# Kernel optimization log

Measured on AMD Instinct MI355X. Metric: run time of the kernel, lower is better.

The kernel has to match this reference:

```python
import jax, jax.numpy as jnp
import numpy as np

# Config (matches init_kwargs)
IN_CH = 128
HID = 128
HEADS = 1
B, H, W = 8, 192, 192


def setup_inputs() -> dict:
    key = jax.random.key(0)
    ks = jax.random.split(key, 10)
    s = 0.05
    x = jax.random.normal(ks[0], (B, IN_CH, H, W), dtype=jnp.float32)
    # 1x1 conv weights stored as (out, in); bias (out,)
    Wq = jax.random.normal(ks[1], (HID, IN_CH), dtype=jnp.float32) * s
    bq = jax.random.normal(ks[2], (HID,), dtype=jnp.float32) * s
    Wk = jax.random.normal(ks[3], (HID, IN_CH), dtype=jnp.float32) * s
    bk = jax.random.normal(ks[4], (HID,), dtype=jnp.float32) * s
    Wv = jax.random.normal(ks[5], (HID, IN_CH), dtype=jnp.float32) * s
    bv = jax.random.normal(ks[6], (HID,), dtype=jnp.float32) * s
    Wo = jax.random.normal(ks[7], (IN_CH, HID), dtype=jnp.float32) * s
    bo = jax.random.normal(ks[8], (IN_CH,), dtype=jnp.float32) * s
    gamma = jax.random.normal(ks[9], (1,), dtype=jnp.float32) * 0.5
    return {"x": x, "Wq": Wq, "bq": bq, "Wk": Wk, "bk": bk,
            "Wv": Wv, "bv": bv, "Wo": Wo, "bo": bo, "gamma": gamma}


def _conv1x1(x, Wt, b):
    # x: (B, Cin, H, W); Wt: (Cout, Cin) -> (B, Cout, H, W)
    return jnp.einsum('oc,bchw->bohw', Wt, x) + b[None, :, None, None]


def reference(x, Wq, bq, Wk, bk, Wv, bv, Wo, bo, gamma):
    b, c, h, w = x.shape
    n = h * w
    d = HID // HEADS
    # q/k/v: (B, hidden, H, W) -> view(B, d, heads, N) -> (B*heads, d, N)
    def proj(Wt, bias):
        y = _conv1x1(x, Wt, bias).reshape(b, d, HEADS, n)
        return jnp.transpose(y, (0, 2, 1, 3)).reshape(b * HEADS, d, n)
    q = proj(Wq, bq)
    k = proj(Wk, bk)
    v = proj(Wv, bv)
    # NOTE: energy is d x d (channel attention), contracted over N. No scale.
    energy = jnp.einsum('bdn,ben->bde', q, k)        # (B*heads, d, d)
    attention = jax.nn.softmax(energy, axis=-1)
    attn_out = jnp.einsum('bde,ben->bdn', attention, v)  # (B*heads, d, N)
    attn_out = attn_out.reshape(b, HEADS, d, n)
    attn_out = jnp.transpose(attn_out, (0, 2, 1, 3)).reshape(b, HID, h, w)
    attn_out = _conv1x1(attn_out, Wo, bo)
    return gamma * attn_out + x
```

## Files before the change

kernel.cpp:

```cpp
#include <hip/hip_runtime.h>
#include <cstdint>
#include <cstddef>

#define NB  8
#define NC  128
#define NHW 36864

#define GOFF  0
#define SOFF  131072
#define TOFF  132096
#define ROFF  133120
#define CVOFF 264192
#define MBOFF 265216

typedef __attribute__((ext_vector_type(8))) short short8;
typedef __attribute__((ext_vector_type(4))) float f32x4;

static __device__ __forceinline__ f32x4 zero4(){ f32x4 v = {0.f,0.f,0.f,0.f}; return v; }

static __device__ __forceinline__ short bfbits(float f){
    union { __bf16 b; short s; } u; u.b = (__bf16)f; return u.s;
}
static __device__ __forceinline__ void cv2(float f, short& hb, short& lb){
    union { __bf16 b; short s; } u;
    u.b = (__bf16)f; hb = u.s;
    float hf = (float)u.b;
    u.b = (__bf16)(f - hf); lb = u.s;
}
static __device__ __forceinline__ float cv8(f32x4 v0, f32x4 v1, short8& h, short8& l){
    float ss = 0.f;
#pragma unroll
    for (int j=0;j<4;j++){
        short hb, lb;
        cv2(v0[j], hb, lb); h[j]   = hb; l[j]   = lb;
        cv2(v1[j], hb, lb); h[4+j] = hb; l[4+j] = lb;
        ss += v0[j] + v1[j];
    }
    return ss;
}

__global__ __launch_bounds__(256) void k_zero(float* __restrict__ p){
    const int i = (blockIdx.x*256 + threadIdx.x)*4;
    *(f32x4*)(p + i) = zero4();
}

#define GNT 36
#define GLDH 5120

__global__ __launch_bounds__(512) void k_gram(const float* __restrict__ x,
                                              float* __restrict__ G,
                                              float* __restrict__ svec){
    __shared__ short Ls[2][2][GLDH];
    const int b     = blockIdx.y;
    const int chunk = blockIdx.x;
    const int tid   = threadIdx.x;
    const int wid   = tid >> 6, lane = tid & 63;
    const int l16   = lane & 15, lgi = lane >> 4;
    const int sr    = tid >> 2;
    const int sc    = (tid & 3) * 8;

    const float* xs = x + (size_t)b*NC*NHW + (size_t)sr*NHW + chunk*1152 + sc;

    float srow = 0.f;
    f32x4 acc[8];
#pragma unroll
    for (int g=0;g<8;g++) acc[g] = zero4();

    const int ra = (wid*16 + l16)*40 + lgi*8;

    {
        f32x4 v0 = *(const f32x4*)(xs);
        f32x4 v1 = *(const f32x4*)(xs+4);
        short8 h0,l0;
        srow += cv8(v0,v1,h0,l0);
        *(short8*)&Ls[0][0][sr*40 + sc] = h0;
        *(short8*)&Ls[0][1][sr*40 + sc] = l0;
    }
    __syncthreads();

    for (int t=0; t<GNT-1; ++t){
        const float* p = xs + (t+1)*32;
        f32x4 v0 = *(const f32x4*)(p);
        f32x4 v1 = *(const f32x4*)(p+4);
        __builtin_amdgcn_sched_barrier(0);

        {
            const short* Lh = Ls[t&1][0];
            const short* Ll = Ls[t&1][1];
            short8 hA = *(const short8*)(Lh + ra);
            short8 lA = *(const short8*)(Ll + ra);
#pragma unroll
            for (int g=0; g<8; g++){
                const int rb = (g*16 + l16)*40 + lgi*8;
                short8 hg  = *(const short8*)(Lh + rb);
                short8 lg2 = *(const short8*)(Ll + rb);
                acc[g] = __builtin_amdgcn_mfma_f32_16x16x32_bf16(hA, hg,  acc[g], 0,0,0);
                acc[g] = __builtin_amdgcn_mfma_f32_16x16x32_bf16(hA, lg2, acc[g], 0,0,0);
                acc[g] = __builtin_amdgcn_mfma_f32_16x16x32_bf16(lA, hg,  acc[g], 0,0,0);
            }
        }

        {
            short8 h0,l0;
            srow += cv8(v0,v1,h0,l0);
            *(short8*)&Ls[(t+1)&1][0][sr*40 + sc] = h0;
            *(short8*)&Ls[(t+1)&1][1][sr*40 + sc] = l0;
        }
        __syncthreads();
    }

    {
        const short* Lh = Ls[(GNT-1)&1][0];
        const short* Ll = Ls[(GNT-1)&1][1];
        short8 hA = *(const short8*)(Lh + ra);
        short8 lA = *(const short8*)(Ll + ra);
#pragma unroll
        for (int g=0; g<8; g++){
            const int rb = (g*16 + l16)*40 + lgi*8;
            short8 hg  = *(const short8*)(Lh + rb);
            short8 lg2 = *(const short8*)(Ll + rb);
            acc[g] = __builtin_amdgcn_mfma_f32_16x16x32_bf16(hA, hg,  acc[g], 0,0,0);
            acc[g] = __builtin_amdgcn_mfma_f32_16x16x32_bf16(hA, lg2, acc[g], 0,0,0);
            acc[g] = __builtin_amdgcn_mfma_f32_16x16x32_bf16(lA, hg,  acc[g], 0,0,0);
        }
    }

    float* Gb = G + (size_t)b*NC*NC;
#pragma unroll
    for (int g=0;g<8;g++){
#pragma unroll
        for (int r=0;r<4;r++){
            atomicAdd(&Gb[(size_t)(wid*16 + lgi*4 + r)*NC + g*16 + l16], acc[g][r]);
        }
    }
    srow += __shfl_xor(srow, 1);
    srow += __shfl_xor(srow, 2);
    if ((tid & 3) == 0) atomicAdd(&svec[b*NC + sr], srow);
}

__global__ __launch_bounds__(256) void k_energyav(const float* __restrict__ G,
        const float* __restrict__ svec,
        const float* __restrict__ Wq, const float* __restrict__ bq,
        const float* __restrict__ Wk, const float* __restrict__ bk,
        const float* __restrict__ bv, const float* __restrict__ Wv,
        float* __restrict__ R, float* __restrict__ tvec){
    const int b  = blockIdx.y;
    const int d0 = blockIdx.x * 16;
    const int tid = threadIdx.x;
    const int d  = tid & 15;
    const int ec = tid >> 4;

    __shared__ float Ps[16][128];
    __shared__ float Es[16][128];
    __shared__ float red[16][16];
    __shared__ float rowmax[16];
    __shared__ float rowsum[16];
    __shared__ float qs[16];

    const float* Wqrow = Wq + (size_t)(d0 + d)*NC;
    const float* sb = svec + b*NC;
#pragma unroll
    for (int i=0;i<8;i++){
        const int c = ec*8 + i;
        const float* Grow = G + ((size_t)b*NC + c)*NC;
        float a = 0.f;
        for (int c4=0;c4<32;c4++){
            f32x4 g4 = *(const f32x4*)(Grow + c4*4);
            f32x4 w4 = *(const f32x4*)(Wqrow + c4*4);
            a += g4[0]*w4[0] + g4[1]*w4[1] + g4[2]*w4[2] + g4[3]*w4[3];
        }
        Ps[d][c] = a;
    }
    if (ec == 0){
        float a = 0.f;
        for (int c4=0;c4<32;c4++){
            f32x4 w4 = *(const f32x4*)(Wqrow + c4*4);
            f32x4 s4 = *(const f32x4*)(sb + c4*4);
            a += w4[0]*s4[0] + w4[1]*s4[1] + w4[2]*s4[2] + w4[3]*s4[3];
        }
        qs[d] = a;
    }
    __syncthreads();
    const float bqd = bq[d0+d];
#pragma unroll
    for (int i=0;i<8;i++){
        const int e = ec*8 + i;
        const float* Wkrow = Wk + (size_t)e*NC;
        float ea = 0.f, ks = 0.f;
        for (int c4=0;c4<32;c4++){
            f32x4 w4 = *(const f32x4*)(Wkrow + c4*4);
            f32x4 p4 = *(const f32x4*)(&Ps[d][c4*4]);
            f32x4 s4 = *(const f32x4*)(sb + c4*4);
            ea += w4[0]*p4[0]+w4[1]*p4[1]+w4[2]*p4[2]+w4[3]*p4[3];
            ks += w4[0]*s4[0]+w4[1]*s4[1]+w4[2]*s4[2]+w4[3]*s4[3];
        }
        const float bke = bk[e];
        Es[d][e] = ea + bke*qs[d] + bqd*ks + (float)NHW*bqd*bke;
    }
    float m8 = -3.4e38f;
#pragma unroll
    for (int i=0;i<8;i++) m8 = fmaxf(m8, Es[d][ec*8+i]);
    red[d][ec] = m8;
    __syncthreads();
    if (tid < 16){
        float m = red[tid][0];
        for (int j=1;j<16;j++) m = fmaxf(m, red[tid][j]);
        rowmax[tid] = m;
    }
    __syncthreads();
    const float rm = rowmax[d];
    float s8 = 0.f;
#pragma unroll
    for (int i=0;i<8;i++){
        float ex = expf(Es[d][ec*8+i] - rm);
        Es[d][ec*8+i] = ex;
        s8 += ex;
    }
    red[d][ec] = s8;
    __syncthreads();
    if (tid < 16){
        float sm = 0.f;
        for (int j=0;j<16;j++) sm += red[tid][j];
        rowsum[tid] = sm;
    }
    __syncthreads();
    const float inv = 1.f / rowsum[d];
    float ta = 0.f;
#pragma unroll
    for (int i=0;i<8;i++){
        const int e = ec*8 + i;
        float av = Es[d][e] * inv;
        Es[d][e] = av;
        ta += av * bv[e];
    }
    red[d][ec] = ta;
    __syncthreads();
    if (tid < 16){
        float sm = 0.f;
        for (int j=0;j<16;j++) sm += red[tid][j];
        tvec[b*NC + d0 + tid] = sm;
    }
    const int c0 = ec*8;
    float racc[8];
#pragma unroll
    for (int i=0;i<8;i++) racc[i]=0.f;
    for (int e=0;e<NC;e++){
        const float av = Es[d][e];
        const float* wv = Wv + (size_t)e*NC + c0;
        f32x4 w0 = *(const f32x4*)wv;
        f32x4 w1 = *(const f32x4*)(wv+4);
        racc[0]+=av*w0[0]; racc[1]+=av*w0[1]; racc[2]+=av*w0[2]; racc[3]+=av*w0[3];
        racc[4]+=av*w1[0]; racc[5]+=av*w1[1]; racc[6]+=av*w1[2]; racc[7]+=av*w1[3];
    }
    float* Rrow = R + ((size_t)b*NC + d0 + d)*NC + c0;
#pragma unroll
    for (int i=0;i<8;i++) Rrow[i] = racc[i];
}

__global__ __launch_bounds__(256) void k_om(const float* __restrict__ R,
        const float* __restrict__ Wo, const float* __restrict__ bo,
        const float* __restrict__ tvec, const float* __restrict__ gamma,
        short* __restrict__ Mb_, float* __restrict__ cvg){
    const int b = blockIdx.y, o0 = blockIdx.x*16;
    const int tid = threadIdx.x, o = tid&15, cc = tid>>4;
    const int c0 = cc*8;
    const float* Worow = Wo + (size_t)(o0+o)*NC;
    const float* tb = tvec + b*NC;
    float a[8];
#pragma unroll
    for (int i=0;i<8;i++) a[i]=0.f;
    float cv = 0.f;
    for (int dd=0; dd<NC; dd++){
        const float wv = Worow[dd];
        const float* r = R + ((size_t)b*NC + dd)*NC + c0;
        f32x4 r0 = *(const f32x4*)r;
        f32x4 r1 = *(const f32x4*)(r+4);
        a[0]+=wv*r0[0]; a[1]+=wv*r0[1]; a[2]+=wv*r0[2]; a[3]+=wv*r0[3];
        a[4]+=wv*r1[0]; a[5]+=wv*r1[1]; a[6]+=wv*r1[2]; a[7]+=wv*r1[3];
        cv += wv*tb[dd];
    }
    const float gm = gamma[0];
    const int c   = o0 + o;
    const int cg  = c >> 4;
    const int kst = cc >> 2, lgv = cc & 3;
    const size_t idx = ((((size_t)b*8 + cg)*4 + kst)*64 + (lgv*16 + (c & 15)))*8;
    short8 hh;
#pragma unroll
    for (int i=0;i<8;i++){
        float val = gm*a[i] + ((c0 + i) == c ? 1.f : 0.f);
        hh[i] = bfbits(val);
    }
    *(short8*)(Mb_ + idx) = hh;
    if (cc == 0) cvg[b*NC + c] = gm*(cv + bo[c]);
}

__global__ __launch_bounds__(256, 4) void k_final(const float* __restrict__ x,
        const short* __restrict__ Mb_, const float* __restrict__ cvg,
        float* __restrict__ out){
    __shared__ short Xt[NC*128];
    const int b   = blockIdx.y;
    const int n0  = blockIdx.x * 128;
    const int tid = threadIdx.x;
    const int wid = tid >> 6, lane = tid & 63;
    const int l16 = lane & 15, lgi = lane >> 4;

    const int nr = tid & 31, mb8 = tid >> 5;
    const float* xs = x + (size_t)b*NC*NHW + n0 + nr*4;
#pragma unroll
    for (int rep=0; rep<2; rep++){
        const int m0 = rep*64 + mb8*8;
        const float* xm = xs + (size_t)m0*NHW;
        f32x4 v0 = *(const f32x4*)(xm);
        f32x4 v1 = *(const f32x4*)(xm + (size_t)1*NHW);
        f32x4 v2 = *(const f32x4*)(xm + (size_t)2*NHW);
        f32x4 v3 = *(const f32x4*)(xm + (size_t)3*NHW);
        f32x4 v4 = *(const f32x4*)(xm + (size_t)4*NHW);
        f32x4 v5 = *(const f32x4*)(xm + (size_t)5*NHW);
        f32x4 v6 = *(const f32x4*)(xm + (size_t)6*NHW);
        f32x4 v7 = *(const f32x4*)(xm + (size_t)7*NHW);
#pragma unroll
        for (int r=0;r<4;r++){
            short8 w;
            w[0]=bfbits(v0[r]); w[1]=bfbits(v1[r]); w[2]=bfbits(v2[r]); w[3]=bfbits(v3[r]);
            w[4]=bfbits(v4[r]); w[5]=bfbits(v5[r]); w[6]=bfbits(v6[r]); w[7]=bfbits(v7[r]);
            const int n = nr*4 + r;
            const int slot = (rep*8 + mb8) ^ ((n>>2)&15) ^ ((n&3)<<2);
            *(short8*)(&Xt[n*128 + slot*8]) = w;
        }
    }
    __syncthreads();

    f32x4 acc[2][8];
#pragma unroll
    for (int t=0;t<2;t++)
#pragma unroll
      for (int g=0;g<8;g++) acc[t][g]=zero4();

    const short* Mb = Mb_ + (size_t)b*16384;

#pragma unroll
    for (int ks=0; ks<4; ks++){
        const int nA0 = wid*32 + l16;
        const int nA1 = nA0 + 16;
        const int sl  = ks*4 + lgi;
        const int s0  = sl ^ ((nA0>>2)&15) ^ ((nA0&3)<<2);
        const int s1  = sl ^ ((nA1>>2)&15) ^ ((nA1&3)<<2);
        short8 a0 = *(const short8*)(&Xt[nA0*128 + s0*8]);
        short8 a1 = *(const short8*)(&Xt[nA1*128 + s1*8]);
#pragma unroll
        for (int cg=0; cg<8; cg++){
            short8 bh = *(const short8*)(Mb + (((size_t)cg*4 + ks)*64 + lane)*8);
            acc[0][cg] = __builtin_amdgcn_mfma_f32_16x16x32_bf16(a0, bh, acc[0][cg], 0,0,0);
            acc[1][cg] = __builtin_amdgcn_mfma_f32_16x16x32_bf16(a1, bh, acc[1][cg], 0,0,0);
        }
    }

    const float* cb = cvg + b*NC;
#pragma unroll
    for (int cg=0;cg<8;cg++){
        const int c = cg*16 + l16;
        const float ccv = cb[c];
        float* orow = &out[((size_t)b*NC + c)*NHW + n0 + wid*32 + lgi*4];
#pragma unroll
        for (int t=0;t<2;t++){
            f32x4 o = acc[t][cg];
            o[0]+=ccv; o[1]+=ccv; o[2]+=ccv; o[3]+=ccv;
            *(f32x4*)(orow + t*16) = o;
        }
    }
}

extern "C" void kernel_launch(void* const* d_in, const int* in_sizes, int n_in,
                              void* d_out, int out_size, void* d_ws, size_t ws_size,
                              hipStream_t stream){
    const float* x     = (const float*)d_in[0];
    const float* Wq    = (const float*)d_in[1];
    const float* bq    = (const float*)d_in[2];
    const float* Wk    = (const float*)d_in[3];
    const float* bk    = (const float*)d_in[4];
    const float* Wv    = (const float*)d_in[5];
    const float* bv    = (const float*)d_in[6];
    const float* Wo    = (const float*)d_in[7];
    const float* bo    = (const float*)d_in[8];
    const float* gamma = (const float*)d_in[9];
    float* out = (float*)d_out;

    float* w  = (float*)d_ws;
    float* G  = w + GOFF;
    float* S  = w + SOFF;
    float* T  = w + TOFF;
    float* R  = w + ROFF;
    float* CV = w + CVOFF;
    short* Mb = (short*)(w + MBOFF);

    k_zero    <<<dim3(129),     256, 0, stream>>>(G);

    k_gram    <<<dim3(32,  NB), 512, 0, stream>>>(x, G, S);
    k_energyav<<<dim3(8,   NB), 256, 0, stream>>>(G, S, Wq, bq, Wk, bk, bv, Wv, R, T);
    k_om      <<<dim3(8,   NB), 256, 0, stream>>>(R, Wo, bo, T, gamma, Mb, CV);
    k_final   <<<dim3(288, NB), 256, 0, stream>>>(x, Mb, CV, out);
}
```

Before: 176.8 us.

## Triple-buffer gram kernel LDS with XOR swizzle and deeper global prefetch

Reworks the gram kernel's main loop from double to triple LDS buffering, unrolled by two, with global loads issued two tiles ahead. The padded row stride of 40 is replaced by an unpadded stride of 32 with an XOR swizzle to avoid bank conflicts. The aim is to hide global load latency behind the MFMA work and shrink the LDS footprint. In exchange it keeps more prefetch registers live and adds more complex buffer rotation logic, which could raise register pressure.

```diff
diff --git a/kernel.cpp b/kernel.cpp
--- a/kernel.cpp
+++ b/kernel.cpp
@@ -45,85 +45,91 @@
 }
 
 #define GNT 36
-#define GLDH 5120
+#define GTS 4096
 
 __global__ __launch_bounds__(512) void k_gram(const float* __restrict__ x,
                                               float* __restrict__ G,
                                               float* __restrict__ svec){
-    __shared__ short Ls[2][2][GLDH];
+    __shared__ short Ls[3][2][GTS];
     const int b     = blockIdx.y;
     const int chunk = blockIdx.x;
     const int tid   = threadIdx.x;
     const int wid   = tid >> 6, lane = tid & 63;
     const int l16   = lane & 15, lgi = lane >> 4;
     const int sr    = tid >> 2;
-    const int sc    = (tid & 3) * 8;
-
-    const float* xs = x + (size_t)b*NC*NHW + (size_t)sr*NHW + chunk*1152 + sc;
+    const int sc8   = (tid & 3) * 8;
+    const int swzW  = ((sr >> 1) & 3) << 3;
+    const int wIdx  = sr*32 + (sc8 ^ swzW);
+
+    const int swzR  = ((l16 >> 1) & 3) << 3;
+    const int cR    = (lgi*8) ^ swzR;
+    const int raOff = (wid*16 + l16)*32 + cR;
+
+    const float* xs = x + (size_t)b*NC*NHW + (size_t)sr*NHW + chunk*1152 + sc8;
 
     float srow = 0.f;
     f32x4 acc[8];
 #pragma unroll
     for (int g=0;g<8;g++) acc[g] = zero4();
 
-    const int ra = (wid*16 + l16)*40 + lgi*8;
+#define GR_STAGE(BUF, V0, V1)  { short8 h0,l0; srow += cv8(V0,V1,h0,l0); \
+        *(short8*)&Ls[BUF][0][wIdx] = h0; *(short8*)&Ls[BUF][1][wIdx] = l0; }
+
+#define GR_COMPUTE(BUF) { \
+        const short* Lh = &Ls[BUF][0][0]; \
+        const short* Ll = &Ls[BUF][1][0]; \
+        short8 hA = *(const short8*)(Lh + raOff); \
+        short8 lA = *(const short8*)(Ll + raOff); \
+        _Pragma("unroll") \
+        for (int g=0; g<8; g++){ \
+            const int rb = (g*16 + l16)*32 + cR; \
+            short8 hg  = *(const short8*)(Lh + rb); \
+            short8 lg2 = *(const short8*)(Ll + rb); \
+            acc[g] = __builtin_amdgcn_mfma_f32_16x16x32_bf16(hA, hg,  acc[g], 0,0,0); \
+            acc[g] = __builtin_amdgcn_mfma_f32_16x16x32_bf16(hA, lg2, acc[g], 0,0,0); \
+            acc[g] = __builtin_amdgcn_mfma_f32_16x16x32_bf16(lA, hg,  acc[g], 0,0,0); \
+        } }
 
     {
         f32x4 v0 = *(const f32x4*)(xs);
         f32x4 v1 = *(const f32x4*)(xs+4);
-        short8 h0,l0;
-        srow += cv8(v0,v1,h0,l0);
-        *(short8*)&Ls[0][0][sr*40 + sc] = h0;
-        *(short8*)&Ls[0][1][sr*40 + sc] = l0;
-    }
-    __syncthreads();
-
-    for (int t=0; t<GNT-1; ++t){
-        const float* p = xs + (t+1)*32;
-        f32x4 v0 = *(const f32x4*)(p);
-        f32x4 v1 = *(const f32x4*)(p+4);
+        GR_STAGE(0, v0, v1);
+        f32x4 u0 = *(const f32x4*)(xs+32);
+        f32x4 u1 = *(const f32x4*)(xs+36);
+        GR_STAGE(1, u0, u1);
+    }
+    f32x4 pA0 = *(const f32x4*)(xs + 64);
+    f32x4 pA1 = *(const f32x4*)(xs + 68);
+    f32x4 pB0, pB1;
+    __syncthreads();
+
+    int bm0 = 0, bm1 = 1, bm2 = 2;
+    for (int tt = 0; tt < GNT-2; tt += 2){
+        {
+            const float* p = xs + (size_t)(tt+3)*32;
+            pB0 = *(const f32x4*)(p);
+            pB1 = *(const f32x4*)(p+4);
+        }
         __builtin_amdgcn_sched_barrier(0);
-
-        {
-            const short* Lh = Ls[t&1][0];
-            const short* Ll = Ls[t&1][1];
-            short8 hA = *(const short8*)(Lh + ra);
-            short8 lA = *(const short8*)(Ll + ra);
-#pragma unroll
-            for (int g=0; g<8; g++){
-                const int rb = (g*16 + l16)*40 + lgi*8;
-                short8 hg  = *(const short8*)(Lh + rb);
-                short8 lg2 = *(const short8*)(Ll + rb);
-                acc[g] = __builtin_amdgcn_mfma_f32_16x16x32_bf16(hA, hg,  acc[g], 0,0,0);
-                acc[g] = __builtin_amdgcn_mfma_f32_16x16x32_bf16(hA, lg2, acc[g], 0,0,0);
-                acc[g] = __builtin_amdgcn_mfma_f32_16x16x32_bf16(lA, hg,  acc[g], 0,0,0);
-            }
-        }
-
-        {
-            short8 h0,l0;
-            srow += cv8(v0,v1,h0,l0);
-            *(short8*)&Ls[(t+1)&1][0][sr*40 + sc] = h0;
-            *(short8*)&Ls[(t+1)&1][1][sr*40 + sc] = l0;
-        }
+        GR_COMPUTE(bm0);
+        GR_STAGE(bm2, pA0, pA1);
         __syncthreads();
-    }
-
-    {
-        const short* Lh = Ls[(GNT-1)&1][0];
-        const short* Ll = Ls[(GNT-1)&1][1];
-        short8 hA = *(const short8*)(Lh + ra);
-        short8 lA = *(const short8*)(Ll + ra);
-#pragma unroll
-        for (int g=0; g<8; g++){
-            const int rb = (g*16 + l16)*40 + lgi*8;
-            short8 hg  = *(const short8*)(Lh + rb);
-            short8 lg2 = *(const short8*)(Ll + rb);
-            acc[g] = __builtin_amdgcn_mfma_f32_16x16x32_bf16(hA, hg,  acc[g], 0,0,0);
-            acc[g] = __builtin_amdgcn_mfma_f32_16x16x32_bf16(hA, lg2, acc[g], 0,0,0);
-            acc[g] = __builtin_amdgcn_mfma_f32_16x16x32_bf16(lA, hg,  acc[g], 0,0,0);
-        }
-    }
+        if (tt+4 < GNT){
+            const float* p = xs + (size_t)(tt+4)*32;
+            pA0 = *(const f32x4*)(p);
+            pA1 = *(const f32x4*)(p+4);
+        }
+        __builtin_amdgcn_sched_barrier(0);
+        GR_COMPUTE(bm1);
+        GR_STAGE(bm0, pB0, pB1);
+        __syncthreads();
+        const int tmp = bm2; bm2 = bm1; bm1 = bm0; bm0 = tmp;
+    }
+    GR_COMPUTE(bm0);
+    GR_COMPUTE(bm1);
+
+#undef GR_STAGE
+#undef GR_COMPUTE
 
     float* Gb = G + (size_t)b*NC*NC;
 #pragma unroll
```

Result: faster. 173.0 us (-2.1%).
